# Optimization experiments

Measured on AMD Instinct MI355X. Metric: run time of the kernel, lower is better.

The kernel has to match this reference:

```python
import jax, jax.numpy as jnp
import numpy as np

B, S, E, H = 4, 2048, 1024, 16
D = E // H  # head_dim = 64


def setup_inputs() -> dict:
    key = jax.random.key(0)
    k1, k2, k3, k4, k5 = jax.random.split(key, 5)
    # xavier_uniform bounds
    lim_qkv = float(np.sqrt(6.0 / (E + 3 * E)))
    lim_out = float(np.sqrt(6.0 / (E + E)))
    return {
        "inp": jax.random.normal(k1, (B, S, E), dtype=jnp.float32),
        "qkv_w": jax.random.uniform(k2, (3 * E, E), minval=-lim_qkv, maxval=lim_qkv, dtype=jnp.float32),
        "qkv_b": jnp.zeros((3 * E,), dtype=jnp.float32),
        "out_w": jax.random.uniform(k3, (E, E), minval=-lim_out, maxval=lim_out, dtype=jnp.float32),
        "out_b": jnp.zeros((E,), dtype=jnp.float32),
    }


def reference(inp, qkv_w, qkv_b, out_w, out_b):
    b, s, _ = inp.shape
    # qkv projection: [b,s,3E]
    qkv = jnp.einsum("bse,fe->bsf", inp, qkv_w) + qkv_b
    qkv = qkv.reshape(b, s, 3, H, D).transpose(2, 0, 3, 1, 4)  # [3,b,h,s,d]
    q, k, v = qkv[0], qkv[1], qkv[2]
    scale = 1.0 / jnp.sqrt(jnp.float32(D))
    scores = jnp.einsum("bhqd,bhkd->bhqk", q, k) * scale
    attn = jax.nn.softmax(scores, axis=-1)  # dropout = identity (eval mode)
    ctx = jnp.einsum("bhqk,bhkd->bhqd", attn, v)
    ctx = ctx.transpose(0, 2, 1, 3).reshape(b, s, E)
    out = jnp.einsum("bse,fe->bsf", ctx, out_w) + out_b
    return out
```

## Files before the change

### kernel.cpp

```cpp
#include <hip/hip_runtime.h>
#include <stdint.h>

typedef unsigned short u16;
typedef __bf16 bf16x8 __attribute__((ext_vector_type(8)));
typedef float f32x4 __attribute__((ext_vector_type(4)));
typedef float f32x16 __attribute__((ext_vector_type(16)));

#define DEV static __device__ __forceinline__

DEV u16 f2bf(float f) {
  uint32_t u = __float_as_uint(f);
  u += 0x7fffu + ((u >> 16) & 1u);
  return (u16)(u >> 16);
}

DEV void g2l16(const void* g, void* l) {
  __builtin_amdgcn_global_load_lds(
      (__attribute__((address_space(1))) void*)(g),
      (__attribute__((address_space(3))) void*)(l), 16, 0, 0);
}

DEV f32x4 mfma16(bf16x8 a, bf16x8 b, f32x4 c) {
  return __builtin_amdgcn_mfma_f32_16x16x32_bf16(a, b, c, 0, 0, 0);
}
DEV f32x16 mfma32(bf16x8 a, bf16x8 b, f32x16 c) {
  return __builtin_amdgcn_mfma_f32_32x32x16_bf16(a, b, c, 0, 0, 0);
}

DEV bf16x8 lds_ld(const char* p) { return *(const bf16x8*)p; }

DEV float fexp2(float x) {
  float r;
  asm("v_exp_f32 %0, %1" : "=v"(r) : "v"(x));
  return r;
}

DEV uint32_t cvtpk(float lo, float hi) {
  uint32_t r;
  asm("v_cvt_pk_bf16_f32 %0, %1, %2" : "=v"(r) : "v"(lo), "v"(hi));
  return r;
}
DEV void pswap(uint32_t& a, uint32_t& b) {
  auto r = __builtin_amdgcn_permlane32_swap((int)a, (int)b, false, false);
  a = (uint32_t)r[0];
  b = (uint32_t)r[1];
}
DEV float xhalf_sum(float x) {
  auto r = __builtin_amdgcn_permlane32_swap(__float_as_int(x), __float_as_int(x), false, false);
  return __int_as_float(r[0]) + __int_as_float(r[1]);
}

__global__ __launch_bounds__(256) void cvt_kernel(const float* __restrict__ in,
                                                  u16* __restrict__ out, int n4) {
  int i = blockIdx.x * 256 + threadIdx.x;
  if (i >= n4) return;
  float4 v = ((const float4*)in)[i];
  ushort4 o;
  o.x = f2bf(v.x); o.y = f2bf(v.y); o.z = f2bf(v.z); o.w = f2bf(v.w);
  ((ushort4*)out)[i] = o;
}

template<int EPI>
__global__ __launch_bounds__(256, 2) void gemm_bt(
    const u16* __restrict__ A, const u16* __restrict__ B,
    const float* __restrict__ bias, void* __restrict__ C,
    int M, int N, int K) {
  __shared__ char sm[2][32768];
  const int tid = threadIdx.x;
  const int w = tid >> 6, l = tid & 63;
  const int wr = w >> 1, wc = w & 1;
  const int bm0 = blockIdx.x * 128, bn0 = blockIdx.y * 128;
  const int lr = l >> 3, lsl = (l & 7) ^ lr;
  const u16* gA = A + (size_t)(bm0 + w * 32 + lr) * K + lsl * 8;
  const u16* gB = B + (size_t)(bn0 + w * 32 + lr) * K + lsl * 8;

  auto stage = [&](int t, int pp) {
    char* ba = sm[pp] + w * 32 * 128;
    char* bb = ba + 16384;
    const u16* a = gA + t * 64;
    const u16* b = gB + t * 64;
#pragma unroll
    for (int i = 0; i < 4; ++i) {
      g2l16(a + (size_t)i * 8 * K, ba + i * 8 * 128);
      g2l16(b + (size_t)i * 8 * K, bb + i * 8 * 128);
    }
  };

  f32x4 acc[4][4] = {};
  const int NT = K / 64;
  int pp = 0;
  stage(0, 0);
  __syncthreads();
  for (int t = 0; t < NT; ++t) {
    if (t + 1 < NT) stage(t + 1, pp ^ 1);
    const char* bufA = sm[pp];
    const char* bufB = bufA + 16384;
#pragma unroll
    for (int ks = 0; ks < 2; ++ks) {
      bf16x8 af[4], bfr[4];
#pragma unroll
      for (int i = 0; i < 4; ++i) {
        const int rowA = wr * 64 + i * 16 + (l & 15);
        const int colb = (ks * 64 + ((l >> 4) << 4)) ^ ((rowA & 7) << 4);
        af[i] = lds_ld(bufA + rowA * 128 + colb);
        const int rowB = wc * 64 + i * 16 + (l & 15);
        bfr[i] = lds_ld(bufB + rowB * 128 + colb);
      }
#pragma unroll
      for (int i = 0; i < 4; ++i)
#pragma unroll
        for (int j = 0; j < 4; ++j)
          acc[i][j] = mfma16(af[i], bfr[j], acc[i][j]);
    }
    __syncthreads();
    pp ^= 1;
  }
  const int cr = (l >> 4) * 4, cc = l & 15;
#pragma unroll
  for (int i = 0; i < 4; ++i) {
    const int gr = bm0 + wr * 64 + i * 16 + cr;
#pragma unroll
    for (int j = 0; j < 4; ++j) {
      const int gc = bn0 + wc * 64 + j * 16 + cc;
      const float bv = bias[gc];
#pragma unroll
      for (int r = 0; r < 4; ++r) {
        const float v = acc[i][j][r] + bv;
        if (EPI == 0) ((float*)C)[(size_t)(gr + r) * N + gc] = v;
        else          ((u16*)C)[(size_t)(gr + r) * N + gc] = f2bf(v);
      }
    }
  }
}

__global__ __launch_bounds__(256) void vtrans(const u16* __restrict__ qkv,
                                              u16* __restrict__ vT) {
  const int st = blockIdx.x, bh = blockIdx.y;
  const int b = bh >> 4, h = bh & 15;
  __shared__ char tile[8192];
  const int t = threadIdx.x;
  const int s = t >> 2, q = t & 3;
  const u16* src = qkv + ((size_t)(b * 2048 + st * 64 + s)) * 3072 + 2048 + h * 64;
#pragma unroll
  for (int i = 0; i < 2; ++i) {
    const int slot = q + i * 4;
    uint4 v = *(const uint4*)(src + slot * 8);
    *(uint4*)(tile + s * 128 + ((slot ^ (s & 7)) * 16)) = v;
  }
  __syncthreads();
  const int d = t >> 2;
#pragma unroll
  for (int i = 0; i < 2; ++i) {
    const int ss0 = (q + i * 4) * 8;
    union { u16 v[8]; uint4 u; } pk;
#pragma unroll
    for (int k = 0; k < 8; ++k) {
      const int ss = ss0 + k;
      pk.v[k] = *(const u16*)(tile + ss * 128 + (((d >> 3) ^ (ss & 7)) * 16) + (d & 7) * 2);
    }
    *(uint4*)(vT + ((size_t)(bh * 64 + d)) * 2048 + st * 64 + ss0) = pk.u;
  }
}

__global__ __launch_bounds__(256, 4) void attn(const u16* __restrict__ qkv,
                                               const u16* __restrict__ vT,
                                               u16* __restrict__ ctx) {
  constexpr int S = 2048, E = 1024, TE = 3072, NT = S / 64;
  const int qt = blockIdx.x, bh = blockIdx.y;
  const int b = bh >> 4, h = bh & 15;
  const int tid = threadIdx.x, w = tid >> 6, l = tid & 63;
  const int q = l & 31, hi = l >> 5;
  __shared__ char sm[2][16384];

  const int qglob = qt * 128 + w * 32 + q;
  const u16* qp = qkv + (size_t)(b * S + qglob) * TE + h * 64 + hi * 8;
  bf16x8 qf[4];
#pragma unroll
  for (int d = 0; d < 4; ++d) qf[d] = *(const bf16x8*)(qp + d * 16);

  const int lr = l >> 3, lsl = (l & 7) ^ lr;
  const u16* gK = qkv + (size_t)(b * S) * TE + E + h * 64 + lsl * 8;
  const u16* gV = vT + (size_t)(bh * 64) * S + lsl * 8;

  auto stage = [&](int t, int pp) {
    char* bk = sm[pp] + w * 2048;
#pragma unroll
    for (int i = 0; i < 2; ++i) {
      const int row = w * 16 + i * 8 + lr;
      g2l16(gK + (size_t)(t * 64 + row) * TE, bk + i * 1024);
      g2l16(gV + (size_t)row * S + t * 64, bk + 8192 + i * 1024);
    }
  };

  f32x16 o0 = {}, o1 = {};
  float lsum = 0.f;
  constexpr float cexp = 0.18033688f;
  constexpr float cbias = -cexp * 12.0f;

  int pp = 0;
  stage(0, 0);
  __syncthreads();
  for (int t = 0; t < NT; ++t) {
    if (t + 1 < NT) stage(t + 1, pp ^ 1);
    const char* bK = sm[pp];
    const char* bV = sm[pp] + 8192;
    const int swz = (q & 7) << 4;
#pragma unroll
    for (int s = 0; s < 2; ++s) {
      const char* kr = bK + (s * 32 + q) * 128;
      f32x16 st = {};
      __builtin_amdgcn_s_setprio(1);
#pragma unroll
      for (int d = 0; d < 4; ++d)
        st = mfma32(lds_ld(kr + (((d * 2 + hi) << 4) ^ swz)), qf[d], st);
      __builtin_amdgcn_s_setprio(0);
      const int s0 = (((s * 4 + hi) << 4) ^ swz);
      const int s1 = (((s * 4 + 2 + hi) << 4) ^ swz);
      const bf16x8 va0 = lds_ld(bV + q * 128 + s0);
      const bf16x8 va1 = lds_ld(bV + q * 128 + s1);
      const bf16x8 vb0 = lds_ld(bV + (32 + q) * 128 + s0);
      const bf16x8 vb1 = lds_ld(bV + (32 + q) * 128 + s1);
      float ts[4] = {0.f, 0.f, 0.f, 0.f};
#pragma unroll
      for (int r = 0; r < 16; ++r) {
        st[r] = fexp2(fmaf(st[r], cexp, cbias));
        ts[r & 3] += st[r];
      }
      lsum += (ts[0] + ts[1]) + (ts[2] + ts[3]);
      uint32_t a0 = cvtpk(st[0], st[1]), c0 = cvtpk(st[4], st[5]);
      uint32_t a1 = cvtpk(st[2], st[3]), c1 = cvtpk(st[6], st[7]);
      pswap(a0, c0); pswap(a1, c1);
      uint32_t a2 = cvtpk(st[8], st[9]), c2 = cvtpk(st[12], st[13]);
      uint32_t a3 = cvtpk(st[10], st[11]), c3 = cvtpk(st[14], st[15]);
      pswap(a2, c2); pswap(a3, c3);
      union { uint32_t u[4]; bf16x8 v; } p0, p1;
      p0.u[0] = a0; p0.u[1] = a1; p0.u[2] = c0; p0.u[3] = c1;
      p1.u[0] = a2; p1.u[1] = a3; p1.u[2] = c2; p1.u[3] = c3;
      __builtin_amdgcn_s_setprio(1);
      o0 = mfma32(va0, p0.v, o0);
      o0 = mfma32(va1, p1.v, o0);
      o1 = mfma32(vb0, p0.v, o1);
      o1 = mfma32(vb1, p1.v, o1);
      __builtin_amdgcn_s_setprio(0);
    }
    __syncthreads();
    pp ^= 1;
  }
  const float inv = 1.0f / xhalf_sum(lsum);
  u16* cp = ctx + (size_t)(b * S + qglob) * E + h * 64 + 4 * hi;
#pragma unroll
  for (int g = 0; g < 4; ++g) {
    ushort4 pk0, pk1;
    pk0.x = f2bf(o0[4 * g + 0] * inv); pk0.y = f2bf(o0[4 * g + 1] * inv);
    pk0.z = f2bf(o0[4 * g + 2] * inv); pk0.w = f2bf(o0[4 * g + 3] * inv);
    *(ushort4*)(cp + 8 * g) = pk0;
    pk1.x = f2bf(o1[4 * g + 0] * inv); pk1.y = f2bf(o1[4 * g + 1] * inv);
    pk1.z = f2bf(o1[4 * g + 2] * inv); pk1.w = f2bf(o1[4 * g + 3] * inv);
    *(ushort4*)(cp + 32 + 8 * g) = pk1;
  }
}

extern "C" void kernel_launch(void* const* d_in, const int* in_sizes, int n_in,
                              void* d_out, int out_size, void* d_ws, size_t ws_size,
                              hipStream_t stream) {
  (void)in_sizes; (void)n_in; (void)out_size;
  const float* inp   = (const float*)d_in[0];
  const float* qkv_w = (const float*)d_in[1];
  const float* qkv_b = (const float*)d_in[2];
  const float* out_w = (const float*)d_in[3];
  const float* out_b = (const float*)d_in[4];
  char* ws = (char*)d_ws;
  if (ws_size < 92274688u) return;

  u16* inp_b  = (u16*)(ws);
  u16* qkvw_b = (u16*)(ws + 16777216);
  u16* outw_b = (u16*)(ws + 23068672);
  u16* qkvo   = (u16*)(ws + 25165824);
  u16* vTb    = (u16*)(ws + 75497472);
  u16* ctx    = inp_b;

  hipLaunchKernelGGL(cvt_kernel, dim3(8192), dim3(256), 0, stream, inp, inp_b, 2097152);
  hipLaunchKernelGGL(cvt_kernel, dim3(3072), dim3(256), 0, stream, qkv_w, qkvw_b, 786432);
  hipLaunchKernelGGL(cvt_kernel, dim3(1024), dim3(256), 0, stream, out_w, outw_b, 262144);
  hipLaunchKernelGGL((gemm_bt<1>), dim3(64, 24), dim3(256), 0, stream,
                     inp_b, qkvw_b, qkv_b, (void*)qkvo, 8192, 3072, 1024);
  hipLaunchKernelGGL(vtrans, dim3(32, 64), dim3(256), 0, stream, qkvo, vTb);
  hipLaunchKernelGGL(attn, dim3(16, 64), dim3(256), 0, stream, qkvo, vTb, ctx);
  hipLaunchKernelGGL((gemm_bt<0>), dim3(64, 8), dim3(256), 0, stream,
                     ctx, outw_b, out_b, d_out, 8192, 1024, 1024);
}
```

Measured before the change: 187.9 us.

## Process two query sub-tiles per warp in attention to reuse K/V fragments

Each warp now handles 64 query rows (two 32-row groups) instead of 32, so every K and V fragment loaded from LDS feeds two sets of MFMAs. The attention grid is halved and launch bounds drop to 2 blocks per SIMD to allow the doubled accumulator and Q registers. This cuts LDS reads and global K/V staging per query, at the cost of higher register pressure, lower occupancy and fewer blocks (512) to cover the GPU.

```diff
diff --git a/kernel.cpp b/kernel.cpp
--- a/kernel.cpp
+++ b/kernel.cpp
@@ -162,7 +162,7 @@
   }
 }
 
-__global__ __launch_bounds__(256, 4) void attn(const u16* __restrict__ qkv,
+__global__ __launch_bounds__(256, 2) void attn(const u16* __restrict__ qkv,
                                                const u16* __restrict__ vT,
                                                u16* __restrict__ ctx) {
   constexpr int S = 2048, E = 1024, TE = 3072, NT = S / 64;
@@ -172,11 +172,16 @@
   const int q = l & 31, hi = l >> 5;
   __shared__ char sm[2][16384];
 
-  const int qglob = qt * 128 + w * 32 + q;
-  const u16* qp = qkv + (size_t)(b * S + qglob) * TE + h * 64 + hi * 8;
-  bf16x8 qf[4];
-#pragma unroll
-  for (int d = 0; d < 4; ++d) qf[d] = *(const bf16x8*)(qp + d * 16);
+  const int qglobA = qt * 256 + w * 64 + q;
+  const int qglobB = qglobA + 32;
+  const u16* qpA = qkv + (size_t)(b * S + qglobA) * TE + h * 64 + hi * 8;
+  const u16* qpB = qkv + (size_t)(b * S + qglobB) * TE + h * 64 + hi * 8;
+  bf16x8 qfA[4], qfB[4];
+#pragma unroll
+  for (int d = 0; d < 4; ++d) {
+    qfA[d] = *(const bf16x8*)(qpA + d * 16);
+    qfB[d] = *(const bf16x8*)(qpB + d * 16);
+  }
 
   const int lr = l >> 3, lsl = (l & 7) ^ lr;
   const u16* gK = qkv + (size_t)(b * S) * TE + E + h * 64 + lsl * 8;
@@ -192,10 +197,32 @@
     }
   };
 
-  f32x16 o0 = {}, o1 = {};
-  float lsum = 0.f;
+  f32x16 o0A = {}, o1A = {}, o0B = {}, o1B = {};
+  float lsumA = 0.f, lsumB = 0.f;
   constexpr float cexp = 0.18033688f;
   constexpr float cbias = -cexp * 12.0f;
+
+  auto expsum = [&](f32x16& e, float& ls) {
+    float ts[4] = {0.f, 0.f, 0.f, 0.f};
+#pragma unroll
+    for (int r = 0; r < 16; ++r) {
+      e[r] = fexp2(fmaf(e[r], cexp, cbias));
+      ts[r & 3] += e[r];
+    }
+    ls += (ts[0] + ts[1]) + (ts[2] + ts[3]);
+  };
+  auto mkfrag = [&](const f32x16& e, bf16x8& P0, bf16x8& P1) {
+    uint32_t a0 = cvtpk(e[0], e[1]), c0 = cvtpk(e[4], e[5]);
+    uint32_t a1 = cvtpk(e[2], e[3]), c1 = cvtpk(e[6], e[7]);
+    pswap(a0, c0); pswap(a1, c1);
+    uint32_t a2 = cvtpk(e[8], e[9]), c2 = cvtpk(e[12], e[13]);
+    uint32_t a3 = cvtpk(e[10], e[11]), c3 = cvtpk(e[14], e[15]);
+    pswap(a2, c2); pswap(a3, c3);
+    union { uint32_t u[4]; bf16x8 v; } t0, t1;
+    t0.u[0] = a0; t0.u[1] = a1; t0.u[2] = c0; t0.u[3] = c1;
+    t1.u[0] = a2; t1.u[1] = a3; t1.u[2] = c2; t1.u[3] = c3;
+    P0 = t0.v; P1 = t1.v;
+  };
 
   int pp = 0;
   stage(0, 0);
@@ -208,11 +235,16 @@
 #pragma unroll
     for (int s = 0; s < 2; ++s) {
       const char* kr = bK + (s * 32 + q) * 128;
-      f32x16 st = {};
+      bf16x8 kf[4];
+#pragma unroll
+      for (int d = 0; d < 4; ++d) kf[d] = lds_ld(kr + (((d * 2 + hi) << 4) ^ swz));
+      f32x16 stA = {}, stB = {};
       __builtin_amdgcn_s_setprio(1);
 #pragma unroll
-      for (int d = 0; d < 4; ++d)
-        st = mfma32(lds_ld(kr + (((d * 2 + hi) << 4) ^ swz)), qf[d], st);
+      for (int d = 0; d < 4; ++d) {
+        stA = mfma32(kf[d], qfA[d], stA);
+        stB = mfma32(kf[d], qfB[d], stB);
+      }
       __builtin_amdgcn_s_setprio(0);
       const int s0 = (((s * 4 + hi) << 4) ^ swz);
       const int s1 = (((s * 4 + 2 + hi) << 4) ^ swz);
@@ -220,44 +252,37 @@
       const bf16x8 va1 = lds_ld(bV + q * 128 + s1);
       const bf16x8 vb0 = lds_ld(bV + (32 + q) * 128 + s0);
       const bf16x8 vb1 = lds_ld(bV + (32 + q) * 128 + s1);
-      float ts[4] = {0.f, 0.f, 0.f, 0.f};
-#pragma unroll
-      for (int r = 0; r < 16; ++r) {
-        st[r] = fexp2(fmaf(st[r], cexp, cbias));
-        ts[r & 3] += st[r];
-      }
-      lsum += (ts[0] + ts[1]) + (ts[2] + ts[3]);
-      uint32_t a0 = cvtpk(st[0], st[1]), c0 = cvtpk(st[4], st[5]);
-      uint32_t a1 = cvtpk(st[2], st[3]), c1 = cvtpk(st[6], st[7]);
-      pswap(a0, c0); pswap(a1, c1);
-      uint32_t a2 = cvtpk(st[8], st[9]), c2 = cvtpk(st[12], st[13]);
-      uint32_t a3 = cvtpk(st[10], st[11]), c3 = cvtpk(st[14], st[15]);
-      pswap(a2, c2); pswap(a3, c3);
-      union { uint32_t u[4]; bf16x8 v; } p0, p1;
-      p0.u[0] = a0; p0.u[1] = a1; p0.u[2] = c0; p0.u[3] = c1;
-      p1.u[0] = a2; p1.u[1] = a3; p1.u[2] = c2; p1.u[3] = c3;
+      expsum(stA, lsumA);
+      expsum(stB, lsumB);
+      bf16x8 pA0, pA1, pB0, pB1;
+      mkfrag(stA, pA0, pA1);
+      mkfrag(stB, pB0, pB1);
       __builtin_amdgcn_s_setprio(1);
-      o0 = mfma32(va0, p0.v, o0);
-      o0 = mfma32(va1, p1.v, o0);
-      o1 = mfma32(vb0, p0.v, o1);
-      o1 = mfma32(vb1, p1.v, o1);
+      o0A = mfma32(va0, pA0, o0A); o0B = mfma32(va0, pB0, o0B);
+      o0A = mfma32(va1, pA1, o0A); o0B = mfma32(va1, pB1, o0B);
+      o1A = mfma32(vb0, pA0, o1A); o1B = mfma32(vb0, pB0, o1B);
+      o1A = mfma32(vb1, pA1, o1A); o1B = mfma32(vb1, pB1, o1B);
       __builtin_amdgcn_s_setprio(0);
     }
     __syncthreads();
     pp ^= 1;
   }
-  const float inv = 1.0f / xhalf_sum(lsum);
-  u16* cp = ctx + (size_t)(b * S + qglob) * E + h * 64 + 4 * hi;
-#pragma unroll
-  for (int g = 0; g < 4; ++g) {
-    ushort4 pk0, pk1;
-    pk0.x = f2bf(o0[4 * g + 0] * inv); pk0.y = f2bf(o0[4 * g + 1] * inv);
-    pk0.z = f2bf(o0[4 * g + 2] * inv); pk0.w = f2bf(o0[4 * g + 3] * inv);
-    *(ushort4*)(cp + 8 * g) = pk0;
-    pk1.x = f2bf(o1[4 * g + 0] * inv); pk1.y = f2bf(o1[4 * g + 1] * inv);
-    pk1.z = f2bf(o1[4 * g + 2] * inv); pk1.w = f2bf(o1[4 * g + 3] * inv);
-    *(ushort4*)(cp + 32 + 8 * g) = pk1;
-  }
+  auto writeo = [&](const f32x16& e0, const f32x16& e1, float ls, int qg) {
+    const float inv = 1.0f / xhalf_sum(ls);
+    u16* cp = ctx + (size_t)(b * S + qg) * E + h * 64 + 4 * hi;
+#pragma unroll
+    for (int g = 0; g < 4; ++g) {
+      ushort4 pk0, pk1;
+      pk0.x = f2bf(e0[4 * g + 0] * inv); pk0.y = f2bf(e0[4 * g + 1] * inv);
+      pk0.z = f2bf(e0[4 * g + 2] * inv); pk0.w = f2bf(e0[4 * g + 3] * inv);
+      *(ushort4*)(cp + 8 * g) = pk0;
+      pk1.x = f2bf(e1[4 * g + 0] * inv); pk1.y = f2bf(e1[4 * g + 1] * inv);
+      pk1.z = f2bf(e1[4 * g + 2] * inv); pk1.w = f2bf(e1[4 * g + 3] * inv);
+      *(ushort4*)(cp + 32 + 8 * g) = pk1;
+    }
+  };
+  writeo(o0A, o1A, lsumA, qglobA);
+  writeo(o0B, o1B, lsumB, qglobB);
 }
 
 extern "C" void kernel_launch(void* const* d_in, const int* in_sizes, int n_in,
@@ -285,7 +310,7 @@
   hipLaunchKernelGGL((gemm_bt<1>), dim3(64, 24), dim3(256), 0, stream,
                      inp_b, qkvw_b, qkv_b, (void*)qkvo, 8192, 3072, 1024);
   hipLaunchKernelGGL(vtrans, dim3(32, 64), dim3(256), 0, stream, qkvo, vTb);
-  hipLaunchKernelGGL(attn, dim3(16, 64), dim3(256), 0, stream, qkvo, vTb, ctx);
+  hipLaunchKernelGGL(attn, dim3(8, 64), dim3(256), 0, stream, qkvo, vTb, ctx);
   hipLaunchKernelGGL((gemm_bt<0>), dim3(64, 8), dim3(256), 0, stream,
                      ctx, outw_b, out_b, d_out, 8192, 1024, 1024);
 }
```

Result: no change. 184.4 us (-1.9%).
